# Performance work log

Hardware: AMD Instinct MI355X
Metric: run time of the kernel (lower is better)

The kernel has to match this reference:

```python
import jax, jax.numpy as jnp
import numpy as np

N = 100000      # nodes
E = 1600000     # edges (avg degree 16)
D = 64          # in_channels == conv widths == lin width
G = 64          # graphs in batch
OUT = 10        # out_channels


def setup_inputs() -> dict:
    key = jax.random.key(0)
    ks = jax.random.split(key, 20)
    s = 0.1
    inp = {
        "x": jax.random.normal(ks[0], (N, D), jnp.float32),
        "edge_index": jax.random.randint(ks[1], (2, E), 0, N, dtype=jnp.int64),
        "batch": jnp.sort(jax.random.randint(ks[2], (N,), 0, G, dtype=jnp.int64)),
    }
    k = 3
    for i in range(3):  # 3 SAGEConv layers: lin_l (Wl, bl) on aggregated, lin_r (Wr, no bias) on root
        inp[f"c{i}_Wl"] = jax.random.normal(ks[k], (D, D), jnp.float32) * s; k += 1
        inp[f"c{i}_bl"] = jnp.zeros((D,), jnp.float32)
        inp[f"c{i}_Wr"] = jax.random.normal(ks[k], (D, D), jnp.float32) * s; k += 1
    inp["l0_W"] = jax.random.normal(ks[k], (D, D), jnp.float32) * s; k += 1
    inp["l0_b"] = jnp.zeros((D,), jnp.float32)
    inp["out_W"] = jax.random.normal(ks[k], (D, OUT), jnp.float32) * s; k += 1
    inp["out_b"] = jnp.zeros((OUT,), jnp.float32)
    return inp


def reference(x, edge_index, batch,
              c0_Wl, c0_bl, c0_Wr,
              c1_Wl, c1_bl, c1_Wr,
              c2_Wl, c2_bl, c2_Wr,
              l0_W, l0_b, out_W, out_b):
    src, dst = edge_index[0], edge_index[1]
    # in-degree of each target node (mean conv aggregation), computed once
    deg = jax.ops.segment_sum(jnp.ones((E,), x.dtype), dst, num_segments=N)
    inv_deg = (1.0 / jnp.maximum(deg, 1.0))[:, None]

    def sage(h, Wl, bl, Wr):
        # gather source features, mean-aggregate at targets, then lin_l(agg) + lin_r(h)
        agg = jax.ops.segment_sum(h[src], dst, num_segments=N) * inv_deg
        return agg @ Wl + bl + h @ Wr

    h = jax.nn.relu(sage(x, c0_Wl, c0_bl, c0_Wr))
    h = jax.nn.relu(sage(h, c1_Wl, c1_bl, c1_Wr))
    h = jax.nn.relu(sage(h, c2_Wl, c2_bl, c2_Wr))

    # global mean pool over graphs
    cnt = jax.ops.segment_sum(jnp.ones((N,), h.dtype), batch, num_segments=G)
    g = jax.ops.segment_sum(h, batch, num_segments=G) / jnp.maximum(cnt, 1.0)[:, None]

    g = jax.nn.relu(g @ l0_W + l0_b)
    return g @ out_W + out_b  # [G, OUT]
```

## Files before the change

### kernel.cpp

```cpp
#include <hip/hip_runtime.h>
#include <hip/hip_fp16.h>

#define WPB 8
#define TPB 4
#define PADK 136
#define BSH 8
#define BNODES 256
#define SC_BLOCKS 256
#define HIST_BLOCKS 256
#define HSTRIDE 512

typedef _Float16 half8 __attribute__((ext_vector_type(8)));
typedef _Float16 half4v __attribute__((ext_vector_type(4)));
typedef float floatx4 __attribute__((ext_vector_type(4)));

__global__ __launch_bounds__(256) void gnn_pre(const int* __restrict__ dst,
                                               int* __restrict__ bkt_cnt, int nbkt, int E,
                                               const int* __restrict__ batch,
                                               float* __restrict__ gcnt, int N,
                                               const float4* __restrict__ xin,
                                               ushort4* __restrict__ x16o, int n4,
                                               __half* __restrict__ x16,
                                               __half* __restrict__ hA,
                                               __half* __restrict__ hB,
                                               int* __restrict__ hist_all) {
    int tid = threadIdx.x;
    if (blockIdx.x < HIST_BLOCKS) {
        __shared__ int h[512];
        __shared__ int gb[64];
        for (int i = tid; i < nbkt; i += 256) h[i] = 0;
        if (tid < 64) gb[tid] = 0;
        __syncthreads();
        const int stride = HIST_BLOCKS * 256;
        if ((E & 3) == 0) {
            const int4* dst4 = (const int4*)dst;
            int E4 = E >> 2;
            for (int e = blockIdx.x * 256 + tid; e < E4; e += stride) {
                int4 d = dst4[e];
                atomicAdd(&h[d.x >> BSH], 1);
                atomicAdd(&h[d.y >> BSH], 1);
                atomicAdd(&h[d.z >> BSH], 1);
                atomicAdd(&h[d.w >> BSH], 1);
            }
        } else {
            for (int e = blockIdx.x * 256 + tid; e < E; e += stride)
                atomicAdd(&h[dst[e] >> BSH], 1);
        }
        for (int i = blockIdx.x * 256 + tid; i < N; i += stride)
            atomicAdd(&gb[batch[i]], 1);
        __syncthreads();
        for (int i = tid; i < nbkt; i += 256) {
            int v = h[i];
            hist_all[blockIdx.x * HSTRIDE + i] = v;
            if (v) atomicAdd(&bkt_cnt[i], v);
        }
        if (tid < 64) {
            int v = gb[tid];
            if (v) atomicAdd(&gcnt[tid], (float)v);
        }
        if (blockIdx.x == 0 && tid < 64) {
            x16[(size_t)N * 64 + tid] = __ushort_as_half((unsigned short)0);
            hA[(size_t)N * 64 + tid] = __ushort_as_half((unsigned short)0);
            hB[(size_t)N * 64 + tid] = __ushort_as_half((unsigned short)0);
        }
    } else {
        int i = (blockIdx.x - HIST_BLOCKS) * 256 + tid;
        if (i < n4) {
            float4 f = xin[i];
            ushort4 o;
            o.x = __half_as_ushort(__float2half(f.x));
            o.y = __half_as_ushort(__float2half(f.y));
            o.z = __half_as_ushort(__float2half(f.z));
            o.w = __half_as_ushort(__float2half(f.w));
            x16o[i] = o;
        }
    }
}

__global__ void gnn_bkt_scan(const int* __restrict__ bkt_cnt, int* __restrict__ bkt_base,
                             int* __restrict__ row_ptr, int nbkt, int N) {
    int lane = threadIdx.x;
    int carry = 0;
    for (int base = 0; base < nbkt; base += 64) {
        int idx = base + lane;
        int v = (idx < nbkt) ? bkt_cnt[idx] : 0;
        int x = v;
#pragma unroll
        for (int off = 1; off < 64; off <<= 1) {
            int y = __shfl_up(x, off);
            if (lane >= off) x += y;
        }
        if (idx < nbkt) bkt_base[idx] = carry + (x - v);
        carry += __shfl(x, 63);
    }
    if (lane == 0) {
        bkt_base[nbkt] = carry;
        row_ptr[N] = carry;
    }
}

__global__ __launch_bounds__(256) void gnn_scan2(const int* __restrict__ hist_all,
                                                 const int* __restrict__ bkt_base,
                                                 int* __restrict__ blk_base_all, int nbkt) {
    int b = blockIdx.x;
    int t = threadIdx.x, lane = t & 63, wv = t >> 6;
    __shared__ int wsum[4];
    int v = hist_all[t * HSTRIDE + b];
    int x = v;
#pragma unroll
    for (int off = 1; off < 64; off <<= 1) {
        int y = __shfl_up(x, off);
        if (lane >= off) x += y;
    }
    if (lane == 63) wsum[wv] = x;
    __syncthreads();
    int wexcl = 0;
    for (int w = 0; w < wv; w++) wexcl += wsum[w];
    blk_base_all[t * HSTRIDE + b] = bkt_base[b] + wexcl + (x - v);
}

__global__ __launch_bounds__(256) void gnn_bkt_scatter(const int* __restrict__ src,
                                                       const int* __restrict__ dst,
                                                       const int* __restrict__ blk_base_all,
                                                       unsigned int* __restrict__ pairs,
                                                       int E, int nbkt) {
    __shared__ int cur[512];
    int tid = threadIdx.x;
    for (int i = tid; i < nbkt; i += 256) cur[i] = blk_base_all[blockIdx.x * HSTRIDE + i];
    __syncthreads();
    const int stride = SC_BLOCKS * 256;
    if ((E & 3) == 0) {
        const int4* dst4 = (const int4*)dst;
        const int4* src4 = (const int4*)src;
        int E4 = E >> 2;
        for (int e = blockIdx.x * 256 + tid; e < E4; e += stride) {
            int4 d = dst4[e];
            int4 s = src4[e];
            int p0 = atomicAdd(&cur[d.x >> BSH], 1);
            pairs[p0] = (unsigned int)s.x | ((unsigned int)(d.x & (BNODES - 1)) << 24);
            int p1 = atomicAdd(&cur[d.y >> BSH], 1);
            pairs[p1] = (unsigned int)s.y | ((unsigned int)(d.y & (BNODES - 1)) << 24);
            int p2 = atomicAdd(&cur[d.z >> BSH], 1);
            pairs[p2] = (unsigned int)s.z | ((unsigned int)(d.z & (BNODES - 1)) << 24);
            int p3 = atomicAdd(&cur[d.w >> BSH], 1);
            pairs[p3] = (unsigned int)s.w | ((unsigned int)(d.w & (BNODES - 1)) << 24);
        }
    } else {
        for (int e = blockIdx.x * 256 + tid; e < E; e += stride) {
            int d = dst[e];
            int b = d >> BSH;
            int p = atomicAdd(&cur[b], 1);
            pairs[p] = (unsigned int)src[e] | ((unsigned int)(d & (BNODES - 1)) << 24);
        }
    }
}

__global__ __launch_bounds__(256) void gnn_bkt_csr(const unsigned int* __restrict__ pairs,
                                                   const int* __restrict__ bkt_base,
                                                   int* __restrict__ row_ptr,
                                                   float* __restrict__ inv_deg,
                                                   int* __restrict__ csr_src, int N) {
    __shared__ int hist[BNODES];
    __shared__ int excl[BNODES];
    __shared__ int cur[BNODES];
    int b = blockIdx.x;
    int base = bkt_base[b];
    int cnt = bkt_base[b + 1] - base;
    int nd0 = b << BSH;
    int tid = threadIdx.x;
    hist[tid] = 0;
    __syncthreads();
    {
        int a0 = (4 - (base & 3)) & 3;
        a0 = min(a0, cnt);
        for (int i = tid; i < a0; i += 256) atomicAdd(&hist[pairs[base + i] >> 24], 1);
        int vcnt = (cnt - a0) >> 2;
        const uint4* p4 = (const uint4*)(pairs + base + a0);
        for (int i = tid; i < vcnt; i += 256) {
            uint4 u = p4[i];
            atomicAdd(&hist[u.x >> 24], 1);
            atomicAdd(&hist[u.y >> 24], 1);
            atomicAdd(&hist[u.z >> 24], 1);
            atomicAdd(&hist[u.w >> 24], 1);
        }
        for (int i = a0 + (vcnt << 2) + tid; i < cnt; i += 256)
            atomicAdd(&hist[pairs[base + i] >> 24], 1);
    }
    __syncthreads();
    if (tid < 64) {
        int carry = 0;
#pragma unroll
        for (int c = 0; c < BNODES; c += 64) {
            int v = hist[c + tid];
            int x = v;
#pragma unroll
            for (int off = 1; off < 64; off <<= 1) {
                int y = __shfl_up(x, off);
                if (tid >= off) x += y;
            }
            excl[c + tid] = carry + (x - v);
            carry += __shfl(x, 63);
        }
    }
    __syncthreads();
    {
        int node = nd0 + tid;
        if (node < N) {
            row_ptr[node] = base + excl[tid];
            int d = hist[tid];
            inv_deg[node] = 1.0f / (float)(d > 1 ? d : 1);
        }
        cur[tid] = excl[tid];
    }
    __syncthreads();
    {
        int a0 = (4 - (base & 3)) & 3;
        a0 = min(a0, cnt);
        for (int i = tid; i < a0; i += 256) {
            unsigned int u = pairs[base + i];
            int pos = atomicAdd(&cur[u >> 24], 1);
            csr_src[base + pos] = (int)(u & 0xFFFFFFu);
        }
        int vcnt = (cnt - a0) >> 2;
        const uint4* p4 = (const uint4*)(pairs + base + a0);
        for (int i = tid; i < vcnt; i += 256) {
            uint4 u = p4[i];
            int pos0 = atomicAdd(&cur[u.x >> 24], 1);
            csr_src[base + pos0] = (int)(u.x & 0xFFFFFFu);
            int pos1 = atomicAdd(&cur[u.y >> 24], 1);
            csr_src[base + pos1] = (int)(u.y & 0xFFFFFFu);
            int pos2 = atomicAdd(&cur[u.z >> 24], 1);
            csr_src[base + pos2] = (int)(u.z & 0xFFFFFFu);
            int pos3 = atomicAdd(&cur[u.w >> 24], 1);
            csr_src[base + pos3] = (int)(u.w & 0xFFFFFFu);
        }
        for (int i = a0 + (vcnt << 2) + tid; i < cnt; i += 256) {
            unsigned int u = pairs[base + i];
            int pos = atomicAdd(&cur[u >> 24], 1);
            csr_src[base + pos] = (int)(u & 0xFFFFFFu);
        }
    }
}

#define LOAD4(eReg, c0, vArr)                                  \
    _Pragma("unroll") for (int c_ = 0; c_ < 4; c_++) {         \
        int sj_ = __shfl(eReg, (c0) + c_ * 4 + quad);          \
        vArr[c_] = hin4v[(size_t)sj_ * 16 + m16];              \
    }
#define ACC4(vArr, accum)                                      \
    _Pragma("unroll") for (int c_ = 0; c_ < 4; c_++) {         \
        accum.x += (float)vArr[c_][0];                         \
        accum.y += (float)vArr[c_][1];                         \
        accum.z += (float)vArr[c_][2];                         \
        accum.w += (float)vArr[c_][3];                         \
    }

#define SAGE_GATHER_BODY                                                        \
    int idxl = r0 + lane;                                                       \
    int rr = (lane <= 8) ? row_ptr[min(idxl, n)] : 0;                           \
    float ig = (lane < 8) ? inv_deg[min(idxl, n - 1)] : 0.0f;                   \
    _Pragma("unroll")                                                           \
    for (int jp = 0; jp < 4; jp++) {         \
        int j2 = jp << 1;                                                       \
        int nd = min(r0 + j2 + hf, n);                                          \
        unsigned u = hin32[(size_t)nd * 32 + col];                              \
        ((unsigned*)(my_in + (lr0 + j2 + hf) * PADK + 64))[col] = u;            \
    }                                                                           \
    int ef[8];                                                                  \
    _Pragma("unroll")                                                           \
    for (int j = 0; j < 8; j++) {                                               \
        int s0 = __shfl(rr, j), s1 = __shfl(rr, j + 1);                         \
        int cb = min(64, s1 - s0);                                              \
        ef[j] = (lane < cb) ? csr_src[s0 + lane] : n;                           \
    }                                                                           \
    _Pragma("unroll")                                                           \
    for (int jp = 0; jp < 4; jp++) {                                            \
        int j2 = jp << 1;                                                       \
        int s0A = __shfl(rr, j2), s1A = __shfl(rr, j2 + 1);                     \
        int s1B = __shfl(rr, j2 + 2);                                           \
        int s0B = s1A;                                                          \
        float idgA = __shfl(ig, j2), idgB = __shfl(ig, j2 + 1);                 \
        int cbA = min(64, s1A - s0A), cbB = min(64, s1B - s0B);                 \
        floatx4 accA = {0.f, 0.f, 0.f, 0.f};                                    \
        floatx4 accB = {0.f, 0.f, 0.f, 0.f};                                    \
        {                                                                       \
            half4v vA[4], vB[4];                                                \
            LOAD4(ef[j2], 0, vA);                                               \
            LOAD4(ef[j2 + 1], 0, vB);                                           \
            ACC4(vA, accA);                                                     \
            ACC4(vB, accB);                                                     \
            LOAD4(ef[j2], 16, vA);                    \
            LOAD4(ef[j2 + 1], 16, vB);                                          \
            ACC4(vA, accA);                                                     \
            ACC4(vB, accB);                                                     \
        }                                                                       \
        if (cbA > 32) {                                           \
            half4v v0[4];                                                       \
            LOAD4(ef[j2], 32, v0);                                              \
            ACC4(v0, accA);                                                     \
            if (cbA > 48) { half4v v1[4]; LOAD4(ef[j2], 48, v1); ACC4(v1, accA); } \
        }                                                                       \
        if (cbB > 32) {                                                         \
            half4v v0[4];                                                       \
            LOAD4(ef[j2 + 1], 32, v0);                                          \
            ACC4(v0, accB);                                                     \
            if (cbB > 48) { half4v v1[4]; LOAD4(ef[j2 + 1], 48, v1); ACC4(v1, accB); } \
        }                                                                       \
        for (int base_ = s0A + 64; base_ < s1A; base_ += 64) {                  \
            int cb = min(64, s1A - base_);                                      \
            int ei = (lane < cb) ? csr_src[base_ + lane] : n;                   \
            for (int i0 = 0; i0 < cb; i0 += 16) {                               \
                half4v vt[4];                                                   \
                LOAD4(ei, i0, vt);                                              \
                ACC4(vt, accA);                                                 \
            }                                                                   \
        }                                                                       \
        for (int base_ = s0B + 64; base_ < s1B; base_ += 64) {                  \
            int cb = min(64, s1B - base_);                                      \
            int ei = (lane < cb) ? csr_src[base_ + lane] : n;                   \
            for (int i0 = 0; i0 < cb; i0 += 16) {                               \
                half4v vt[4];                                                   \
                LOAD4(ei, i0, vt);                                              \
                ACC4(vt, accB);                                                 \
            }                                                                   \
        }                                                                       \
        accA.x += __shfl_xor(accA.x, 16); accA.y += __shfl_xor(accA.y, 16);     \
        accA.z += __shfl_xor(accA.z, 16); accA.w += __shfl_xor(accA.w, 16);     \
        accA.x += __shfl_xor(accA.x, 32); accA.y += __shfl_xor(accA.y, 32);     \
        accA.z += __shfl_xor(accA.z, 32); accA.w += __shfl_xor(accA.w, 32);     \
        accB.x += __shfl_xor(accB.x, 16); accB.y += __shfl_xor(accB.y, 16);     \
        accB.z += __shfl_xor(accB.z, 16); accB.w += __shfl_xor(accB.w, 16);     \
        accB.x += __shfl_xor(accB.x, 32); accB.y += __shfl_xor(accB.y, 32);     \
        accB.z += __shfl_xor(accB.z, 32); accB.w += __shfl_xor(accB.w, 32);     \
        if (quad == 0) {                                                        \
            half4v hw;                                                          \
            hw[0] = (_Float16)(accA.x * idgA);                                  \
            hw[1] = (_Float16)(accA.y * idgA);                                  \
            hw[2] = (_Float16)(accA.z * idgA);                                  \
            hw[3] = (_Float16)(accA.w * idgA);                                  \
            *(half4v*)(my_in + (lr0 + j2) * PADK + m16 * 4) = hw;               \
        } else if (quad == 1) {                                                 \
            half4v hw;                                                          \
            hw[0] = (_Float16)(accB.x * idgB);                                  \
            hw[1] = (_Float16)(accB.y * idgB);                                  \
            hw[2] = (_Float16)(accB.z * idgB);                                  \
            hw[3] = (_Float16)(accB.w * idgB);                                  \
            *(half4v*)(my_in + (lr0 + j2 + 1) * PADK + m16 * 4) = hw;           \
        }                                                                       \
    }

__global__ __launch_bounds__(512, 8) void gnn_sage(const __half* __restrict__ hin,
                                                   __half* __restrict__ hout,
                                                   const int* __restrict__ row_ptr,
                                                   const int* __restrict__ csr_src,
                                                   const float* __restrict__ inv_deg,
                                                   const float* __restrict__ Wl,
                                                   const float* __restrict__ bl,
                                                   const float* __restrict__ Wr, int n) {
    __shared__ _Float16 w_lds[64 * PADK];
    __shared__ _Float16 in_lds[TPB][16 * PADK];
    int tid = threadIdx.x, lane = tid & 63, wvid = tid >> 6;
    for (int i = tid; i < 64 * 64; i += 512) {
        int k = i >> 6, nn = i & 63;
        w_lds[nn * PADK + k] = (_Float16)Wl[i];
        w_lds[nn * PADK + 64 + k] = (_Float16)Wr[i];
    }
    __syncthreads();
    int ngroups = (n + 15) >> 4;
    int m16 = lane & 15, quad = lane >> 4;
    int hf = lane >> 5, col = lane & 31;
    const unsigned* hin32 = (const unsigned*)hin;
    const half4v* hin4v = (const half4v*)hin;
    {
        int tg = wvid >> 1, half = wvid & 1;
        int g = blockIdx.x * TPB + tg;
        if (g < ngroups) {
            _Float16* my_in = in_lds[tg];
            int nd0 = g << 4;
            int lr0 = half << 3;
            int r0 = nd0 + lr0;
            SAGE_GATHER_BODY
        }
    }
    __syncthreads();
    int gm = blockIdx.x * TPB + wvid;
    if (wvid < TPB && gm < ngroups) {
        _Float16* my_in = in_lds[wvid];
        int nd0 = gm << 4;
        float bias[4];
#pragma unroll
        for (int nt = 0; nt < 4; nt++) bias[nt] = bl[nt * 16 + m16];
        half8 afrag[4];
        const _Float16* abase = my_in + m16 * PADK + quad * 8;
#pragma unroll
        for (int ks = 0; ks < 4; ks++) afrag[ks] = *(const half8*)(abase + ks * 32);
        floatx4 accv[4];
#pragma unroll
        for (int nt = 0; nt < 4; nt++) {
            accv[nt].x = 0.f; accv[nt].y = 0.f; accv[nt].z = 0.f; accv[nt].w = 0.f;
        }
#pragma unroll
        for (int nt = 0; nt < 4; nt++) {
            const _Float16* bbase = w_lds + (nt * 16 + m16) * PADK + quad * 8;
#pragma unroll
            for (int ks = 0; ks < 4; ks++) {
                half8 bfrag = *(const half8*)(bbase + ks * 32);
                accv[nt] = __builtin_amdgcn_mfma_f32_16x16x32_f16(afrag[ks], bfrag, accv[nt], 0, 0, 0);
            }
        }
#pragma unroll
        for (int nt = 0; nt < 4; nt++) {
#pragma unroll
            for (int r = 0; r < 4; r++) {
                int node = nd0 + quad * 4 + r;
                if (node < n) {
                    float v = fmaxf(accv[nt][r] + bias[nt], 0.0f);
                    hout[(size_t)node * 64 + nt * 16 + m16] = __float2half(v);
                }
            }
        }
    }
}

__global__ __launch_bounds__(512, 8) void gnn_sage_pool(const __half* __restrict__ hin,
                                                        const int* __restrict__ row_ptr,
                                                        const int* __restrict__ csr_src,
                                                        const float* __restrict__ inv_deg,
                                                        const float* __restrict__ Wl,
                                                        const float* __restrict__ bl,
                                                        const float* __restrict__ Wr,
                                                        const int* __restrict__ batch,
                                                        float* __restrict__ gsum, int n) {
    __shared__ _Float16 w_lds[64 * PADK];
    __shared__ _Float16 in_lds[TPB][16 * PADK];
    int tid = threadIdx.x, lane = tid & 63, wvid = tid >> 6;
    for (int i = tid; i < 64 * 64; i += 512) {
        int k = i >> 6, nn = i & 63;
        w_lds[nn * PADK + k] = (_Float16)Wl[i];
        w_lds[nn * PADK + 64 + k] = (_Float16)Wr[i];
    }
    __syncthreads();
    int ngroups = (n + 15) >> 4;
    int m16 = lane & 15, quad = lane >> 4;
    int hf = lane >> 5, col = lane & 31;
    const unsigned* hin32 = (const unsigned*)hin;
    const half4v* hin4v = (const half4v*)hin;
    {
        int tg = wvid >> 1, half = wvid & 1;
        int g = blockIdx.x * TPB + tg;
        if (g < ngroups) {
            _Float16* my_in = in_lds[tg];
            int nd0 = g << 4;
            int lr0 = half << 3;
            int r0 = nd0 + lr0;
            SAGE_GATHER_BODY
        }
    }
    __syncthreads();
    int gm = blockIdx.x * TPB + wvid;
    if (wvid < TPB && gm < ngroups) {
        _Float16* my_in = in_lds[wvid];
        int nd0 = gm << 4;
        float bias[4];
#pragma unroll
        for (int nt = 0; nt < 4; nt++) bias[nt] = bl[nt * 16 + m16];
        half8 afrag[4];
        const _Float16* abase = my_in + m16 * PADK + quad * 8;
#pragma unroll
        for (int ks = 0; ks < 4; ks++) afrag[ks] = *(const half8*)(abase + ks * 32);
        floatx4 accv[4];
#pragma unroll
        for (int nt = 0; nt < 4; nt++) {
            accv[nt].x = 0.f; accv[nt].y = 0.f; accv[nt].z = 0.f; accv[nt].w = 0.f;
        }
#pragma unroll
        for (int nt = 0; nt < 4; nt++) {
            const _Float16* bbase = w_lds + (nt * 16 + m16) * PADK + quad * 8;
#pragma unroll
            for (int ks = 0; ks < 4; ks++) {
                half8 bfrag = *(const half8*)(bbase + ks * 32);
                accv[nt] = __builtin_amdgcn_mfma_f32_16x16x32_f16(afrag[ks], bfrag, accv[nt], 0, 0, 0);
            }
        }
        int bFirst = batch[nd0];
        int bLast = batch[min(nd0 + 15, n - 1)];
        if (bFirst == bLast && nd0 + 15 < n) {
#pragma unroll
            for (int nt = 0; nt < 4; nt++) {
                float s = fmaxf(accv[nt][0] + bias[nt], 0.0f) + fmaxf(accv[nt][1] + bias[nt], 0.0f) +
                          fmaxf(accv[nt][2] + bias[nt], 0.0f) + fmaxf(accv[nt][3] + bias[nt], 0.0f);
                s += __shfl_xor(s, 16);
                s += __shfl_xor(s, 32);
                if (quad == 0) atomicAdd(&gsum[bFirst * 64 + nt * 16 + m16], s);
            }
        } else {
#pragma unroll
            for (int nt = 0; nt < 4; nt++) {
#pragma unroll
                for (int r = 0; r < 4; r++) {
                    int node = nd0 + quad * 4 + r;
                    if (node < n) {
                        int bg = batch[node];
                        float v = fmaxf(accv[nt][r] + bias[nt], 0.0f);
                        atomicAdd(&gsum[bg * 64 + nt * 16 + m16], v);
                    }
                }
            }
        }
    }
}

__global__ __launch_bounds__(1024) void gnn_head(const float* __restrict__ gsum,
                                                 const float* __restrict__ gcnt,
                                                 const float* __restrict__ l0W,
                                                 const float* __restrict__ l0b,
                                                 const float* __restrict__ outW,
                                                 const float* __restrict__ outb,
                                                 float* __restrict__ out, int G, int OUT) {
    __shared__ float gm[64 * 64];
    __shared__ float t2[64 * 64];
    int tid = threadIdx.x;
    for (int i = tid; i < G * 64; i += 1024) {
        int r = i >> 6;
        gm[i] = gsum[i] / fmaxf(gcnt[r], 1.0f);
    }
    __syncthreads();
    for (int i = tid; i < G * 64; i += 1024) {
        int r = i >> 6, c = i & 63;
        float s = l0b[c];
#pragma unroll 8
        for (int k = 0; k < 64; k++) s += gm[(r << 6) + k] * l0W[(k << 6) + c];
        t2[i] = fmaxf(s, 0.0f);
    }
    __syncthreads();
    for (int i = tid; i < G * OUT; i += 1024) {
        int r = i / OUT, c = i - r * OUT;
        float s = outb[c];
#pragma unroll 8
        for (int k = 0; k < 64; k++) s += t2[(r << 6) + k] * outW[k * OUT + c];
        out[i] = s;
    }
}

extern "C" void kernel_launch(void* const* d_in, const int* in_sizes, int n_in,
                              void* d_out, int out_size, void* d_ws, size_t ws_size,
                              hipStream_t stream) {
    const float* x = (const float*)d_in[0];
    const int* ei = (const int*)d_in[1];
    const int* batch = (const int*)d_in[2];
    const float* Wl[3] = {(const float*)d_in[3], (const float*)d_in[6], (const float*)d_in[9]};
    const float* bl[3] = {(const float*)d_in[4], (const float*)d_in[7], (const float*)d_in[10]};
    const float* Wr[3] = {(const float*)d_in[5], (const float*)d_in[8], (const float*)d_in[11]};
    const float* l0W = (const float*)d_in[12];
    const float* l0b = (const float*)d_in[13];
    const float* outW = (const float*)d_in[14];
    const float* outb = (const float*)d_in[15];

    int N = in_sizes[2];
    int E = in_sizes[1] / 2;
    int OUT = 10;
    int G = out_size / OUT;
    const int* src = ei;
    const int* dst = ei + E;
    int NBKT = (N + BNODES - 1) >> BSH;

    char* ws = (char*)d_ws;
    size_t off = 0;
    auto alloc = [&](size_t b) -> char* {
        char* p = ws + off;
        off = (off + b + 255) & ~(size_t)255;
        return p;
    };
    int* row_ptr = (int*)alloc((size_t)(N + 1) * 4);
    int* csr_src = (int*)alloc((size_t)E * 4);
    float* inv_deg = (float*)alloc((size_t)N * 4);
    size_t zoff = off;
    int* bkt_cnt = (int*)alloc((size_t)NBKT * 4);
    float* gcnt = (float*)alloc((size_t)G * 4);
    float* gsum = (float*)alloc((size_t)G * 64 * 4);
    size_t zlen = off - zoff;
    int* bkt_base = (int*)alloc((size_t)(NBKT + 1) * 4);
    int* hist_all = (int*)alloc((size_t)HIST_BLOCKS * HSTRIDE * 4);
    int* blk_base_all = (int*)alloc((size_t)HIST_BLOCKS * HSTRIDE * 4);
    unsigned int* pairs = (unsigned int*)alloc((size_t)E * 4);
    __half* x16 = (__half*)alloc((size_t)(N + 1) * 64 * 2);
    __half* hA = (__half*)alloc((size_t)(N + 1) * 64 * 2);
    __half* hB = (__half*)alloc((size_t)(N + 1) * 64 * 2);

    hipMemsetAsync(ws + zoff, 0, zlen, stream);

    int n4 = N * 64 / 4;
    int pre_blocks = HIST_BLOCKS + (n4 + 255) / 256;
    gnn_pre<<<pre_blocks, 256, 0, stream>>>(dst, bkt_cnt, NBKT, E, batch, gcnt, N,
                                            (const float4*)x, (ushort4*)x16, n4,
                                            x16, hA, hB, hist_all);
    gnn_bkt_scan<<<1, 64, 0, stream>>>(bkt_cnt, bkt_base, row_ptr, NBKT, N);
    gnn_scan2<<<NBKT, 256, 0, stream>>>(hist_all, bkt_base, blk_base_all, NBKT);
    gnn_bkt_scatter<<<SC_BLOCKS, 256, 0, stream>>>(src, dst, blk_base_all, pairs, E, NBKT);
    gnn_bkt_csr<<<NBKT, 256, 0, stream>>>(pairs, bkt_base, row_ptr, inv_deg, csr_src, N);

    int ngroups = (N + 15) >> 4;
    int sage_blocks = (ngroups + TPB - 1) / TPB;
    gnn_sage<<<sage_blocks, 512, 0, stream>>>(x16, hA, row_ptr, csr_src, inv_deg,
                                              Wl[0], bl[0], Wr[0], N);
    gnn_sage<<<sage_blocks, 512, 0, stream>>>(hA, hB, row_ptr, csr_src, inv_deg,
                                              Wl[1], bl[1], Wr[1], N);
    gnn_sage_pool<<<sage_blocks, 512, 0, stream>>>(hB, row_ptr, csr_src, inv_deg,
                                                   Wl[2], bl[2], Wr[2], batch, gsum, N);

    gnn_head<<<1, 1024, 0, stream>>>(gsum, gcnt, l0W, l0b, outW, outb, (float*)d_out, G, OUT);
}
```

Before: 311.4 us.

## Fold bucket scan into scan2, stage pairs in LDS for CSR build, relax launch bounds

Removes the single-block bucket-scan kernel: each scan2 block now computes its own bucket base by reducing the preceding bucket counts, and the last block writes the totals. The CSR build kernel copies each bucket's pairs into a 48KB LDS buffer during the histogram pass and reads them back from LDS for the scatter pass, so the second global read of pairs is avoided. The SAGE kernels' launch-bounds occupancy hint drops from 8 to 4, giving the compiler more registers. Risks: the redundant prefix sums in scan2 grow with the bucket index, the large LDS staging lowers CSR-kernel occupancy, and the register change may hurt latency hiding in the gather-heavy SAGE kernels.

```diff
diff --git a/kernel.cpp b/kernel.cpp
--- a/kernel.cpp
+++ b/kernel.cpp
@@ -1,7 +1,6 @@
 #include <hip/hip_runtime.h>
 #include <hip/hip_fp16.h>
 
-#define WPB 8
 #define TPB 4
 #define PADK 136
 #define BSH 8
@@ -9,6 +8,7 @@
 #define SC_BLOCKS 256
 #define HIST_BLOCKS 256
 #define HSTRIDE 512
+#define PSTAGE 12288
 
 typedef _Float16 half8 __attribute__((ext_vector_type(8)));
 typedef _Float16 half4v __attribute__((ext_vector_type(4)));
@@ -77,34 +77,21 @@
     }
 }
 
-__global__ void gnn_bkt_scan(const int* __restrict__ bkt_cnt, int* __restrict__ bkt_base,
-                             int* __restrict__ row_ptr, int nbkt, int N) {
-    int lane = threadIdx.x;
-    int carry = 0;
-    for (int base = 0; base < nbkt; base += 64) {
-        int idx = base + lane;
-        int v = (idx < nbkt) ? bkt_cnt[idx] : 0;
-        int x = v;
-#pragma unroll
-        for (int off = 1; off < 64; off <<= 1) {
-            int y = __shfl_up(x, off);
-            if (lane >= off) x += y;
-        }
-        if (idx < nbkt) bkt_base[idx] = carry + (x - v);
-        carry += __shfl(x, 63);
-    }
-    if (lane == 0) {
-        bkt_base[nbkt] = carry;
-        row_ptr[N] = carry;
-    }
-}
-
 __global__ __launch_bounds__(256) void gnn_scan2(const int* __restrict__ hist_all,
-                                                 const int* __restrict__ bkt_base,
-                                                 int* __restrict__ blk_base_all, int nbkt) {
+                                                 const int* __restrict__ bkt_cnt,
+                                                 int* __restrict__ bkt_base,
+                                                 int* __restrict__ row_ptr,
+                                                 int* __restrict__ blk_base_all,
+                                                 int nbkt, int N) {
     int b = blockIdx.x;
     int t = threadIdx.x, lane = t & 63, wv = t >> 6;
     __shared__ int wsum[4];
+    __shared__ int red[4];
+    int part = 0;
+    for (int i = t; i < b; i += 256) part += bkt_cnt[i];
+#pragma unroll
+    for (int off = 1; off < 64; off <<= 1) part += __shfl_xor(part, off);
+    if (lane == 0) red[wv] = part;
     int v = hist_all[t * HSTRIDE + b];
     int x = v;
 #pragma unroll
@@ -114,9 +101,18 @@
     }
     if (lane == 63) wsum[wv] = x;
     __syncthreads();
+    int base = red[0] + red[1] + red[2] + red[3];
     int wexcl = 0;
     for (int w = 0; w < wv; w++) wexcl += wsum[w];
-    blk_base_all[t * HSTRIDE + b] = bkt_base[b] + wexcl + (x - v);
+    blk_base_all[t * HSTRIDE + b] = base + wexcl + (x - v);
+    if (t == 0) {
+        bkt_base[b] = base;
+        if (b == nbkt - 1) {
+            int tot = base + bkt_cnt[b];
+            bkt_base[nbkt] = tot;
+            row_ptr[N] = tot;
+        }
+    }
 }
 
 __global__ __launch_bounds__(256) void gnn_bkt_scatter(const int* __restrict__ src,
@@ -163,6 +159,7 @@
     __shared__ int hist[BNODES];
     __shared__ int excl[BNODES];
     __shared__ int cur[BNODES];
+    __shared__ unsigned int pstage[PSTAGE];
     int b = blockIdx.x;
     int base = bkt_base[b];
     int cnt = bkt_base[b + 1] - base;
@@ -170,22 +167,14 @@
     int tid = threadIdx.x;
     hist[tid] = 0;
     __syncthreads();
-    {
-        int a0 = (4 - (base & 3)) & 3;
-        a0 = min(a0, cnt);
-        for (int i = tid; i < a0; i += 256) atomicAdd(&hist[pairs[base + i] >> 24], 1);
-        int vcnt = (cnt - a0) >> 2;
-        const uint4* p4 = (const uint4*)(pairs + base + a0);
-        for (int i = tid; i < vcnt; i += 256) {
-            uint4 u = p4[i];
-            atomicAdd(&hist[u.x >> 24], 1);
-            atomicAdd(&hist[u.y >> 24], 1);
-            atomicAdd(&hist[u.z >> 24], 1);
-            atomicAdd(&hist[u.w >> 24], 1);
-        }
-        for (int i = a0 + (vcnt << 2) + tid; i < cnt; i += 256)
-            atomicAdd(&hist[pairs[base + i] >> 24], 1);
-    }
+    int scnt = min(cnt, PSTAGE);
+    for (int i = tid; i < scnt; i += 256) {
+        unsigned int u = pairs[base + i];
+        pstage[i] = u;
+        atomicAdd(&hist[u >> 24], 1);
+    }
+    for (int i = scnt + tid; i < cnt; i += 256)
+        atomicAdd(&hist[pairs[base + i] >> 24], 1);
     __syncthreads();
     if (tid < 64) {
         int carry = 0;
@@ -213,32 +202,15 @@
         cur[tid] = excl[tid];
     }
     __syncthreads();
-    {
-        int a0 = (4 - (base & 3)) & 3;
-        a0 = min(a0, cnt);
-        for (int i = tid; i < a0; i += 256) {
-            unsigned int u = pairs[base + i];
-            int pos = atomicAdd(&cur[u >> 24], 1);
-            csr_src[base + pos] = (int)(u & 0xFFFFFFu);
-        }
-        int vcnt = (cnt - a0) >> 2;
-        const uint4* p4 = (const uint4*)(pairs + base + a0);
-        for (int i = tid; i < vcnt; i += 256) {
-            uint4 u = p4[i];
-            int pos0 = atomicAdd(&cur[u.x >> 24], 1);
-            csr_src[base + pos0] = (int)(u.x & 0xFFFFFFu);
-            int pos1 = atomicAdd(&cur[u.y >> 24], 1);
-            csr_src[base + pos1] = (int)(u.y & 0xFFFFFFu);
-            int pos2 = atomicAdd(&cur[u.z >> 24], 1);
-            csr_src[base + pos2] = (int)(u.z & 0xFFFFFFu);
-            int pos3 = atomicAdd(&cur[u.w >> 24], 1);
-            csr_src[base + pos3] = (int)(u.w & 0xFFFFFFu);
-        }
-        for (int i = a0 + (vcnt << 2) + tid; i < cnt; i += 256) {
-            unsigned int u = pairs[base + i];
-            int pos = atomicAdd(&cur[u >> 24], 1);
-            csr_src[base + pos] = (int)(u & 0xFFFFFFu);
-        }
+    for (int i = tid; i < scnt; i += 256) {
+        unsigned int u = pstage[i];
+        int pos = atomicAdd(&cur[u >> 24], 1);
+        csr_src[base + pos] = (int)(u & 0xFFFFFFu);
+    }
+    for (int i = scnt + tid; i < cnt; i += 256) {
+        unsigned int u = pairs[base + i];
+        int pos = atomicAdd(&cur[u >> 24], 1);
+        csr_src[base + pos] = (int)(u & 0xFFFFFFu);
     }
 }
 
@@ -349,7 +321,7 @@
         }                                                                       \
     }
 
-__global__ __launch_bounds__(512, 8) void gnn_sage(const __half* __restrict__ hin,
+__global__ __launch_bounds__(512, 4) void gnn_sage(const __half* __restrict__ hin,
                                                    __half* __restrict__ hout,
                                                    const int* __restrict__ row_ptr,
                                                    const int* __restrict__ csr_src,
@@ -422,7 +394,7 @@
     }
 }
 
-__global__ __launch_bounds__(512, 8) void gnn_sage_pool(const __half* __restrict__ hin,
+__global__ __launch_bounds__(512, 4) void gnn_sage_pool(const __half* __restrict__ hin,
                                                         const int* __restrict__ row_ptr,
                                                         const int* __restrict__ csr_src,
                                                         const float* __restrict__ inv_deg,
@@ -594,8 +566,8 @@
     gnn_pre<<<pre_blocks, 256, 0, stream>>>(dst, bkt_cnt, NBKT, E, batch, gcnt, N,
                                             (const float4*)x, (ushort4*)x16, n4,
                                             x16, hA, hB, hist_all);
-    gnn_bkt_scan<<<1, 64, 0, stream>>>(bkt_cnt, bkt_base, row_ptr, NBKT, N);
-    gnn_scan2<<<NBKT, 256, 0, stream>>>(hist_all, bkt_base, blk_base_all, NBKT);
+    gnn_scan2<<<NBKT, 256, 0, stream>>>(hist_all, bkt_cnt, bkt_base, row_ptr,
+                                        blk_base_all, NBKT, N);
     gnn_bkt_scatter<<<SC_BLOCKS, 256, 0, stream>>>(src, dst, blk_base_all, pairs, E, NBKT);
     gnn_bkt_csr<<<NBKT, 256, 0, stream>>>(pairs, bkt_base, row_ptr, inv_deg, csr_src, N);
 
```

Result: faster. 290.1 us (-6.8%).
